# Kernel tuning notes

Measured on AMD Instinct MI355X. Metric: run time of the kernel, lower is better.

The kernel has to match this reference:

```python
import jax, jax.numpy as jnp
import numpy as np

HT_H, HT_W = 512, 512          # Hough accumulator grid
SPHERE_SIZE = 32768            # Gaussian-sphere bins
NUM_VOTES = 1_500_000          # rows in vote_mapping
BATCH, CHANNEL = 2, 64         # channel % 4 == 0 required by the module


def setup_inputs() -> dict:
    key = jax.random.key(0)
    k1, k2, k3, k4 = jax.random.split(key, 4)
    x = jax.random.normal(k1, (BATCH, CHANNEL, HT_H, HT_W), dtype=jnp.float32)
    ht_idx = jax.random.randint(k2, (NUM_VOTES,), 0, HT_H * HT_W, dtype=jnp.int32)
    sphere_idx = jax.random.randint(k3, (NUM_VOTES,), 0, SPHERE_SIZE, dtype=jnp.int32)
    weight = jax.random.uniform(k4, (NUM_VOTES,), dtype=jnp.float32)
    return {"x": x, "ht_idx": ht_idx, "sphere_idx": sphere_idx, "weight": weight}


def reference(x, ht_idx, sphere_idx, weight):
    b, c, h, w = x.shape
    # SPHERE_CUDA.forward: split channels into 4 groups, flatten HT grid
    xf = x.reshape(b * 4, c // 4, h * w)              # [B4, C4, HW]
    # HT2SPHERE: gather each vote's HT cell, scale by vote weight,
    # scatter-add into its sphere bin.
    votes = xf[:, :, ht_idx] * weight                  # [B4, C4, V]
    out = jax.ops.segment_sum(
        jnp.moveaxis(votes, -1, 0), sphere_idx, num_segments=SPHERE_SIZE
    )                                                  # [S, B4, C4]
    out = jnp.moveaxis(out, 0, -1)                     # [B4, C4, S]
    return out.reshape(b, c, SPHERE_SIZE)              # [B, C, S]
```

## Files before the change

### kernel.cpp

```cpp
#include <hip/hip_runtime.h>
#include <stdint.h>


#define S_BINS   32768
#define NBUCKET  1024
#define BINS     32
#define CAP      2048
#define CHUNK    8192
#define HT_BITS  18
#define CUR_STRIDE 16

__device__ __forceinline__ unsigned bf16_rne(float f) {
    unsigned u = __float_as_uint(f);
    return (u + 0x7FFFu + ((u >> 16) & 1u)) >> 16;
}

__global__ void init_kernel(int* __restrict__ cursor, int* __restrict__ spillCnt) {
    const int t = threadIdx.x;
    cursor[t * CUR_STRIDE] = t * CAP;
    if (t == 0) *spillCnt = 0;
}

__global__ __launch_bounds__(512) void fused_tr_kernel(
    const float* __restrict__ x, uint32_t* __restrict__ xTb, int HW,
    const int* __restrict__ ht, const int* __restrict__ sp,
    const float* __restrict__ w, int* __restrict__ cursor,
    uint2* __restrict__ records, uint2* __restrict__ spillRec,
    int* __restrict__ spillBkt, int* __restrict__ spillCnt,
    int V, int nrb) {
    __shared__ __align__(16) char smem[77888];
    const int t = threadIdx.x;
    if ((int)blockIdx.x < nrb) {
        uint2* rec   = (uint2*)smem;
        int*   hist  = (int*)(smem + 65536);
        int*   cur   = (int*)(smem + 69632);
        int*   gbase = (int*)(smem + 73728);
        int*   wsum  = (int*)(smem + 77824);
        const int blk = blockIdx.x;
        const int lane = t & 63, wv = t >> 6;
        const int base = blk * CHUNK, end = min(V, base + CHUNK), n = end - base;
        hist[2 * t] = 0; hist[2 * t + 1] = 0;
        __syncthreads();
        for (int v = base + t; v < end; v += 512) atomicAdd(&hist[sp[v] >> 5], 1);
        __syncthreads();
        const int l0 = hist[2 * t], l1 = hist[2 * t + 1];
        const int tot = l0 + l1;
        int sc = tot;
#pragma unroll
        for (int off = 1; off < 64; off <<= 1) {
            const int up = __shfl_up(sc, off);
            if (lane >= off) sc += up;
        }
        if (lane == 63) wsum[wv] = sc;
        __syncthreads();
        if (wv == 0 && lane < 8) {
            const int v0 = wsum[lane];
            int s = v0;
#pragma unroll
            for (int off = 1; off < 8; off <<= 1) {
                const int up = __shfl_up(s, off);
                if (lane >= off) s += up;
            }
            wsum[lane] = s - v0;
        }
        __syncthreads();
        const int run = wsum[wv] + (sc - tot);
        cur[2 * t]     = run;
        cur[2 * t + 1] = run + l0;
        if (l0) gbase[2 * t]     = atomicAdd(&cursor[(2 * t)     * CUR_STRIDE], l0);
        if (l1) gbase[2 * t + 1] = atomicAdd(&cursor[(2 * t + 1) * CUR_STRIDE], l1);
        __syncthreads();
        for (int v = base + t; v < end; v += 512) {
            const int s = sp[v];
            const int b = s >> 5, sl = s & 31;
            const int pos = atomicAdd(&cur[b], 1);
            rec[pos] = make_uint2((unsigned)ht[v] | ((unsigned)sl << HT_BITS),
                                  __float_as_uint(w[v]));
        }
        __syncthreads();
        for (int i = t; i < n; i += 512) {
            int lo = 0, hi = NBUCKET - 1;
#pragma unroll
            for (int it = 0; it < 10; ++it) {
                const int mid = (lo + hi) >> 1;
                if (i < cur[mid]) hi = mid; else lo = mid + 1;
            }
            const int b = lo;
            const int sb = (b == 0) ? 0 : cur[b - 1];
            const int slot = gbase[b] + (i - sb);
            if (slot < (b + 1) * CAP) {
                records[slot] = rec[i];
            } else {
                const int pos = atomicAdd(spillCnt, 1);
                spillRec[pos] = rec[i];
                spillBkt[pos] = b;
            }
        }
    } else {
        float* tile = (float*)smem;
        const int ht0 = ((int)blockIdx.x - nrb) * 64;
        for (int e = t; e < 128 * 64; e += 512) {
            const int ch = e >> 6, hl = e & 63;
            tile[hl * 129 + ch] = x[(size_t)ch * HW + ht0 + hl];
        }
        __syncthreads();
        for (int e = t; e < 64 * 64; e += 512) {
            const int hl = e >> 6, cp = e & 63;
            const unsigned lo = bf16_rne(tile[hl * 129 + cp]);
            const unsigned hi = bf16_rne(tile[hl * 129 + cp + 64]);
            xTb[(size_t)(ht0 + hl) * 64 + cp] = lo | (hi << 16);
        }
    }
}

__global__ __launch_bounds__(512) void accum_kernel(
    const uint32_t* __restrict__ xTb, const uint2* __restrict__ records,
    const int* __restrict__ cursor, const uint2* __restrict__ spillRec,
    const int* __restrict__ spillBkt, const int* __restrict__ spillCnt,
    float* __restrict__ out) {
    __shared__ uint2 sorted[CAP];
    __shared__ __align__(16) char rawbuf[BINS * 129 * 4];
    __shared__ int hist[BINS], off[BINS + 1], cur[BINS];
    uint2* raw = (uint2*)rawbuf;
    const uint4* xTb4 = (const uint4*)xTb;
    const int bkt = blockIdx.x, t = threadIdx.x;
    const int lane = t & 63, wv = t >> 6;
    const int q = lane >> 4, ql = lane & 15;
    const int n = min(cursor[bkt * CUR_STRIDE] - bkt * CAP, CAP);
    const int rbase = bkt * CAP;
    float a[4][8];
#pragma unroll
    for (int i = 0; i < 4; ++i)
#pragma unroll
        for (int j = 0; j < 8; ++j) a[i][j] = 0.f;

    if (t < BINS) hist[t] = 0;
    __syncthreads();
    for (int i = t; i < n; i += 512) {
        const uint2 r = records[rbase + i];
        raw[i] = r;
        atomicAdd(&hist[(r.x >> HT_BITS) & 31], 1);
    }
    __syncthreads();
    if (t == 0) {
        int run = 0;
        for (int j = 0; j < BINS; ++j) { off[j] = run; cur[j] = run; run += hist[j]; }
        off[BINS] = run;
    }
    __syncthreads();
    for (int i = t; i < n; i += 512) {
        const uint2 r = raw[i];
        const int pos = atomicAdd(&cur[(r.x >> HT_BITS) & 31], 1);
        sorted[pos] = r;
    }
    __syncthreads();
#pragma unroll
    for (int bb = 0; bb < 4; ++bb) {
        const int f = wv * 4 + bb;
        const int s0 = off[f], s1 = off[f + 1];
#pragma unroll 1
        for (int k = s0; k < s1; k += 16) {
#pragma unroll
            for (int u = 0; u < 4; ++u) {
                const int kk = k + 4 * u + q;
                if (kk < s1) {
                    const uint2 r = sorted[kk];
                    const uint4 g = xTb4[(size_t)(r.x & 0x3FFFF) * 16 + ql];
                    const float wt = __uint_as_float(r.y);
                    a[bb][0] += __uint_as_float(g.x << 16)          * wt;
                    a[bb][1] += __uint_as_float(g.x & 0xFFFF0000u)  * wt;
                    a[bb][2] += __uint_as_float(g.y << 16)          * wt;
                    a[bb][3] += __uint_as_float(g.y & 0xFFFF0000u)  * wt;
                    a[bb][4] += __uint_as_float(g.z << 16)          * wt;
                    a[bb][5] += __uint_as_float(g.z & 0xFFFF0000u)  * wt;
                    a[bb][6] += __uint_as_float(g.w << 16)          * wt;
                    a[bb][7] += __uint_as_float(g.w & 0xFFFF0000u)  * wt;
                }
            }
        }
    }
#pragma unroll
    for (int bb = 0; bb < 4; ++bb)
#pragma unroll
        for (int j = 0; j < 8; ++j) {
            a[bb][j] += __shfl_xor(a[bb][j], 16);
            a[bb][j] += __shfl_xor(a[bb][j], 32);
        }
    __syncthreads();
    float* epi = (float*)rawbuf;
    if (lane < 16) {
#pragma unroll
        for (int bb = 0; bb < 4; ++bb) {
            const int f = wv * 4 + bb;
            epi[f * 129 + 4 * ql]      = a[bb][0];
            epi[f * 129 + 4 * ql + 64] = a[bb][1];
            epi[f * 129 + 4 * ql + 1]  = a[bb][2];
            epi[f * 129 + 4 * ql + 65] = a[bb][3];
            epi[f * 129 + 4 * ql + 2]  = a[bb][4];
            epi[f * 129 + 4 * ql + 66] = a[bb][5];
            epi[f * 129 + 4 * ql + 3]  = a[bb][6];
            epi[f * 129 + 4 * ql + 67] = a[bb][7];
        }
    }
    __syncthreads();
    const int cnt = *spillCnt;
    if (cnt > 0) {
        const uint2* xTb2 = (const uint2*)xTb;
        const int hl = lane & 31;
        for (int i = t >> 5; i < cnt; i += 16) {
            if (spillBkt[i] == bkt) {
                const uint2 r = spillRec[i];
                const int f = (r.x >> HT_BITS) & 31;
                const uint2 g = xTb2[(size_t)(r.x & 0x3FFFF) * 32 + hl];
                const float wt = __uint_as_float(r.y);
                atomicAdd(&epi[f * 129 + 2 * hl],
                          __uint_as_float(g.x << 16) * wt);
                atomicAdd(&epi[f * 129 + 2 * hl + 64],
                          __uint_as_float(g.x & 0xFFFF0000u) * wt);
                atomicAdd(&epi[f * 129 + 2 * hl + 1],
                          __uint_as_float(g.y << 16) * wt);
                atomicAdd(&epi[f * 129 + 2 * hl + 65],
                          __uint_as_float(g.y & 0xFFFF0000u) * wt);
            }
        }
        __syncthreads();
    }
    for (int i = t; i < 128 * BINS; i += 512) {
        const int ch = i >> 5, bin = i & 31;
        out[(size_t)ch * S_BINS + bkt * BINS + bin] = epi[bin * 129 + ch];
    }
}

__global__ void direct_kernel(const float* __restrict__ x,
                              const int* __restrict__ ht_idx,
                              const int* __restrict__ sp_idx,
                              const float* __restrict__ weight,
                              float* __restrict__ out, int V, int HW, int S,
                              int CH) {
    const int v = blockIdx.x * 2 + (threadIdx.x >> 7);
    if (v >= V) return;
    const int ch = threadIdx.x & 127;
    if (ch >= CH) return;
    atomicAdd(&out[(size_t)ch * S + sp_idx[v]],
              x[(size_t)ch * HW + ht_idx[v]] * weight[v]);
}

extern "C" void kernel_launch(void* const* d_in, const int* in_sizes, int n_in,
                              void* d_out, int out_size, void* d_ws, size_t ws_size,
                              hipStream_t stream) {
    const float* x  = (const float*)d_in[0];
    const int*   ht = (const int*)d_in[1];
    const int*   sp = (const int*)d_in[2];
    const float* w  = (const float*)d_in[3];
    float* out = (float*)d_out;

    const int HW = 512 * 512;
    const int CH = in_sizes[0] / HW;
    const int S  = out_size / CH;
    const int V  = in_sizes[1];
    const int nrb = (V + CHUNK - 1) / CHUNK;
    const int ntb = HW / 64;

    const size_t xTb_bytes = (size_t)CH * HW * sizeof(uint16_t);
    const size_t rec_bytes = (size_t)NBUCKET * CAP * sizeof(uint2);
    const size_t spr_bytes = (size_t)V * sizeof(uint2);
    const size_t spb_bytes = (size_t)V * sizeof(int);
    const size_t cur_bytes = (size_t)NBUCKET * CUR_STRIDE * sizeof(int);
    const size_t cnt_bytes = 64;
    const size_t need = xTb_bytes + rec_bytes + spr_bytes + spb_bytes +
                        cur_bytes + cnt_bytes;

    if (CH == 128 && S == S_BINS && HW == (1 << HT_BITS) && ws_size >= need) {
        char* p = (char*)d_ws;
        uint32_t* xTb  = (uint32_t*)p;  p += xTb_bytes;
        uint2* records = (uint2*)p;     p += rec_bytes;
        uint2* spillRec= (uint2*)p;     p += spr_bytes;
        int* spillBkt  = (int*)p;       p += spb_bytes;
        int* cursor    = (int*)p;       p += cur_bytes;
        int* spillCnt  = (int*)p;

        init_kernel<<<1, NBUCKET, 0, stream>>>(cursor, spillCnt);
        fused_tr_kernel<<<nrb + ntb, 512, 0, stream>>>(
            x, xTb, HW, ht, sp, w, cursor, records, spillRec, spillBkt,
            spillCnt, V, nrb);
        accum_kernel<<<NBUCKET, 512, 0, stream>>>(xTb, records, cursor,
                                                  spillRec, spillBkt, spillCnt,
                                                  out);
    } else {
        hipMemsetAsync(out, 0, (size_t)out_size * sizeof(float), stream);
        direct_kernel<<<(V + 1) / 2, 256, 0, stream>>>(x, ht, sp, w, out, V, HW,
                                                       S, CH);
    }
}
```

Before: 299.4 us.

## Replace global bucket cursors with per-block sorted chunks gathered in accum

```diff
diff --git a/kernel.cpp b/kernel.cpp
--- a/kernel.cpp
+++ b/kernel.cpp
@@ -7,43 +7,34 @@
 #define BINS     32
 #define CAP      2048
 #define CHUNK    8192
+#define MAXRB    192
 #define HT_BITS  18
-#define CUR_STRIDE 16
 
 __device__ __forceinline__ unsigned bf16_rne(float f) {
     unsigned u = __float_as_uint(f);
     return (u + 0x7FFFu + ((u >> 16) & 1u)) >> 16;
 }
 
-__global__ void init_kernel(int* __restrict__ cursor, int* __restrict__ spillCnt) {
-    const int t = threadIdx.x;
-    cursor[t * CUR_STRIDE] = t * CAP;
-    if (t == 0) *spillCnt = 0;
-}
-
 __global__ __launch_bounds__(512) void fused_tr_kernel(
     const float* __restrict__ x, uint32_t* __restrict__ xTb, int HW,
     const int* __restrict__ ht, const int* __restrict__ sp,
-    const float* __restrict__ w, int* __restrict__ cursor,
-    uint2* __restrict__ records, uint2* __restrict__ spillRec,
-    int* __restrict__ spillBkt, int* __restrict__ spillCnt,
+    const float* __restrict__ w,
+    uint2* __restrict__ records, int* __restrict__ blkcur,
     int V, int nrb) {
-    __shared__ __align__(16) char smem[77888];
+    __shared__ __align__(16) char smem[69696];
     const int t = threadIdx.x;
     if ((int)blockIdx.x < nrb) {
-        uint2* rec   = (uint2*)smem;
-        int*   hist  = (int*)(smem + 65536);
-        int*   cur   = (int*)(smem + 69632);
-        int*   gbase = (int*)(smem + 73728);
-        int*   wsum  = (int*)(smem + 77824);
+        uint2* rec  = (uint2*)smem;
+        int*   hcur = (int*)(smem + 65536);
+        int*   wsum = (int*)(smem + 69632);
         const int blk = blockIdx.x;
         const int lane = t & 63, wv = t >> 6;
         const int base = blk * CHUNK, end = min(V, base + CHUNK), n = end - base;
-        hist[2 * t] = 0; hist[2 * t + 1] = 0;
-        __syncthreads();
-        for (int v = base + t; v < end; v += 512) atomicAdd(&hist[sp[v] >> 5], 1);
-        __syncthreads();
-        const int l0 = hist[2 * t], l1 = hist[2 * t + 1];
+        hcur[2 * t] = 0; hcur[2 * t + 1] = 0;
+        __syncthreads();
+        for (int v = base + t; v < end; v += 512) atomicAdd(&hcur[sp[v] >> 5], 1);
+        __syncthreads();
+        const int l0 = hcur[2 * t], l1 = hcur[2 * t + 1];
         const int tot = l0 + l1;
         int sc = tot;
 #pragma unroll
@@ -65,69 +56,59 @@
         }
         __syncthreads();
         const int run = wsum[wv] + (sc - tot);
-        cur[2 * t]     = run;
-        cur[2 * t + 1] = run + l0;
-        if (l0) gbase[2 * t]     = atomicAdd(&cursor[(2 * t)     * CUR_STRIDE], l0);
-        if (l1) gbase[2 * t + 1] = atomicAdd(&cursor[(2 * t + 1) * CUR_STRIDE], l1);
+        hcur[2 * t]     = run;
+        hcur[2 * t + 1] = run + l0;
         __syncthreads();
         for (int v = base + t; v < end; v += 512) {
             const int s = sp[v];
             const int b = s >> 5, sl = s & 31;
-            const int pos = atomicAdd(&cur[b], 1);
+            const int pos = atomicAdd(&hcur[b], 1);
             rec[pos] = make_uint2((unsigned)ht[v] | ((unsigned)sl << HT_BITS),
                                   __float_as_uint(w[v]));
         }
         __syncthreads();
-        for (int i = t; i < n; i += 512) {
-            int lo = 0, hi = NBUCKET - 1;
-#pragma unroll
-            for (int it = 0; it < 10; ++it) {
-                const int mid = (lo + hi) >> 1;
-                if (i < cur[mid]) hi = mid; else lo = mid + 1;
-            }
-            const int b = lo;
-            const int sb = (b == 0) ? 0 : cur[b - 1];
-            const int slot = gbase[b] + (i - sb);
-            if (slot < (b + 1) * CAP) {
-                records[slot] = rec[i];
-            } else {
-                const int pos = atomicAdd(spillCnt, 1);
-                spillRec[pos] = rec[i];
-                spillBkt[pos] = b;
-            }
-        }
+        for (int i = t; i < n; i += 512)
+            records[(size_t)blk * CHUNK + i] = rec[i];
+        blkcur[(size_t)blk * NBUCKET + 2 * t]     = hcur[2 * t];
+        blkcur[(size_t)blk * NBUCKET + 2 * t + 1] = hcur[2 * t + 1];
     } else {
         float* tile = (float*)smem;
         const int ht0 = ((int)blockIdx.x - nrb) * 64;
-        for (int e = t; e < 128 * 64; e += 512) {
-            const int ch = e >> 6, hl = e & 63;
-            tile[hl * 129 + ch] = x[(size_t)ch * HW + ht0 + hl];
-        }
-        __syncthreads();
-        for (int e = t; e < 64 * 64; e += 512) {
-            const int hl = e >> 6, cp = e & 63;
-            const unsigned lo = bf16_rne(tile[hl * 129 + cp]);
-            const unsigned hi = bf16_rne(tile[hl * 129 + cp + 64]);
-            xTb[(size_t)(ht0 + hl) * 64 + cp] = lo | (hi << 16);
+        for (int e = t; e < 128 * 16; e += 512) {
+            const int ch = e >> 4, hq = e & 15;
+            const float4 v = *(const float4*)(x + (size_t)ch * HW + ht0 + 4 * hq);
+            const int a = 4 * hq;
+            tile[(a + 0) * 129 + ch] = v.x;
+            tile[(a + 1) * 129 + ch] = v.y;
+            tile[(a + 2) * 129 + ch] = v.z;
+            tile[(a + 3) * 129 + ch] = v.w;
+        }
+        __syncthreads();
+        for (int e = t; e < 64 * 32; e += 512) {
+            const int hl = e >> 5, cp = (e & 31) * 2;
+            const unsigned lo0 = bf16_rne(tile[hl * 129 + cp]);
+            const unsigned hi0 = bf16_rne(tile[hl * 129 + cp + 64]);
+            const unsigned lo1 = bf16_rne(tile[hl * 129 + cp + 1]);
+            const unsigned hi1 = bf16_rne(tile[hl * 129 + cp + 65]);
+            *(uint2*)(xTb + (size_t)(ht0 + hl) * 64 + cp) =
+                make_uint2(lo0 | (hi0 << 16), lo1 | (hi1 << 16));
         }
     }
 }
 
 __global__ __launch_bounds__(512) void accum_kernel(
     const uint32_t* __restrict__ xTb, const uint2* __restrict__ records,
-    const int* __restrict__ cursor, const uint2* __restrict__ spillRec,
-    const int* __restrict__ spillBkt, const int* __restrict__ spillCnt,
-    float* __restrict__ out) {
+    const int* __restrict__ blkcur, int nrb, float* __restrict__ out) {
     __shared__ uint2 sorted[CAP];
     __shared__ __align__(16) char rawbuf[BINS * 129 * 4];
     __shared__ int hist[BINS], off[BINS + 1], cur[BINS];
+    __shared__ int segcnt[MAXRB], segpos[MAXRB];
+    __shared__ int ntot;
     uint2* raw = (uint2*)rawbuf;
     const uint4* xTb4 = (const uint4*)xTb;
     const int bkt = blockIdx.x, t = threadIdx.x;
     const int lane = t & 63, wv = t >> 6;
     const int q = lane >> 4, ql = lane & 15;
-    const int n = min(cursor[bkt * CUR_STRIDE] - bkt * CAP, CAP);
-    const int rbase = bkt * CAP;
     float a[4][8];
 #pragma unroll
     for (int i = 0; i < 4; ++i)
@@ -135,11 +116,43 @@
         for (int j = 0; j < 8; ++j) a[i][j] = 0.f;
 
     if (t < BINS) hist[t] = 0;
-    __syncthreads();
-    for (int i = t; i < n; i += 512) {
-        const uint2 r = records[rbase + i];
-        raw[i] = r;
-        atomicAdd(&hist[(r.x >> HT_BITS) & 31], 1);
+    int s0 = 0;
+    if (t < nrb) {
+        const int e1 = blkcur[(size_t)t * NBUCKET + bkt];
+        s0 = (bkt == 0) ? 0 : blkcur[(size_t)t * NBUCKET + bkt - 1];
+        segcnt[t] = e1 - s0;
+    }
+    __syncthreads();
+    if (wv == 0) {
+        int carry = 0;
+        for (int b0 = 0; b0 < nrb; b0 += 64) {
+            const int idx = b0 + lane;
+            const int c = (idx < nrb) ? segcnt[idx] : 0;
+            int sc = c;
+#pragma unroll
+            for (int off2 = 1; off2 < 64; off2 <<= 1) {
+                const int up = __shfl_up(sc, off2);
+                if (lane >= off2) sc += up;
+            }
+            if (idx < nrb) segpos[idx] = carry + sc - c;
+            carry += __shfl(sc, 63);
+        }
+        if (lane == 0) ntot = carry;
+    }
+    __syncthreads();
+    const int n = min(ntot, CAP);
+    if (t < nrb) {
+        const int cnt = segcnt[t];
+        const int p = segpos[t];
+        const uint2* src = records + (size_t)t * CHUNK + s0;
+        for (int j = 0; j < cnt; ++j) {
+            const int d = p + j;
+            if (d < CAP) {
+                const uint2 r = src[j];
+                raw[d] = r;
+                atomicAdd(&hist[(r.x >> HT_BITS) & 31], 1);
+            }
+        }
     }
     __syncthreads();
     if (t == 0) {
@@ -157,13 +170,13 @@
 #pragma unroll
     for (int bb = 0; bb < 4; ++bb) {
         const int f = wv * 4 + bb;
-        const int s0 = off[f], s1 = off[f + 1];
+        const int s0f = off[f], s1f = off[f + 1];
 #pragma unroll 1
-        for (int k = s0; k < s1; k += 16) {
+        for (int k = s0f; k < s1f; k += 16) {
 #pragma unroll
             for (int u = 0; u < 4; ++u) {
                 const int kk = k + 4 * u + q;
-                if (kk < s1) {
+                if (kk < s1f) {
                     const uint2 r = sorted[kk];
                     const uint4 g = xTb4[(size_t)(r.x & 0x3FFFF) * 16 + ql];
                     const float wt = __uint_as_float(r.y);
@@ -203,28 +216,6 @@
         }
     }
     __syncthreads();
-    const int cnt = *spillCnt;
-    if (cnt > 0) {
-        const uint2* xTb2 = (const uint2*)xTb;
-        const int hl = lane & 31;
-        for (int i = t >> 5; i < cnt; i += 16) {
-            if (spillBkt[i] == bkt) {
-                const uint2 r = spillRec[i];
-                const int f = (r.x >> HT_BITS) & 31;
-                const uint2 g = xTb2[(size_t)(r.x & 0x3FFFF) * 32 + hl];
-                const float wt = __uint_as_float(r.y);
-                atomicAdd(&epi[f * 129 + 2 * hl],
-                          __uint_as_float(g.x << 16) * wt);
-                atomicAdd(&epi[f * 129 + 2 * hl + 64],
-                          __uint_as_float(g.x & 0xFFFF0000u) * wt);
-                atomicAdd(&epi[f * 129 + 2 * hl + 1],
-                          __uint_as_float(g.y << 16) * wt);
-                atomicAdd(&epi[f * 129 + 2 * hl + 65],
-                          __uint_as_float(g.y & 0xFFFF0000u) * wt);
-            }
-        }
-        __syncthreads();
-    }
     for (int i = t; i < 128 * BINS; i += 512) {
         const int ch = i >> 5, bin = i & 31;
         out[(size_t)ch * S_BINS + bkt * BINS + bin] = epi[bin * 129 + ch];
@@ -262,29 +253,20 @@
     const int ntb = HW / 64;
 
     const size_t xTb_bytes = (size_t)CH * HW * sizeof(uint16_t);
-    const size_t rec_bytes = (size_t)NBUCKET * CAP * sizeof(uint2);
-    const size_t spr_bytes = (size_t)V * sizeof(uint2);
-    const size_t spb_bytes = (size_t)V * sizeof(int);
-    const size_t cur_bytes = (size_t)NBUCKET * CUR_STRIDE * sizeof(int);
-    const size_t cnt_bytes = 64;
-    const size_t need = xTb_bytes + rec_bytes + spr_bytes + spb_bytes +
-                        cur_bytes + cnt_bytes;
-
-    if (CH == 128 && S == S_BINS && HW == (1 << HT_BITS) && ws_size >= need) {
+    const size_t rec_bytes = (size_t)MAXRB * CHUNK * sizeof(uint2);
+    const size_t cur_bytes = (size_t)MAXRB * NBUCKET * sizeof(int);
+    const size_t need = xTb_bytes + rec_bytes + cur_bytes;
+
+    if (CH == 128 && S == S_BINS && HW == (1 << HT_BITS) && nrb <= MAXRB &&
+        ws_size >= need) {
         char* p = (char*)d_ws;
         uint32_t* xTb  = (uint32_t*)p;  p += xTb_bytes;
         uint2* records = (uint2*)p;     p += rec_bytes;
-        uint2* spillRec= (uint2*)p;     p += spr_bytes;
-        int* spillBkt  = (int*)p;       p += spb_bytes;
-        int* cursor    = (int*)p;       p += cur_bytes;
-        int* spillCnt  = (int*)p;
-
-        init_kernel<<<1, NBUCKET, 0, stream>>>(cursor, spillCnt);
+        int* blkcur    = (int*)p;
+
         fused_tr_kernel<<<nrb + ntb, 512, 0, stream>>>(
-            x, xTb, HW, ht, sp, w, cursor, records, spillRec, spillBkt,
-            spillCnt, V, nrb);
-        accum_kernel<<<NBUCKET, 512, 0, stream>>>(xTb, records, cursor,
-                                                  spillRec, spillBkt, spillCnt,
+            x, xTb, HW, ht, sp, w, records, blkcur, V, nrb);
+        accum_kernel<<<NBUCKET, 512, 0, stream>>>(xTb, records, blkcur, nrb,
                                                   out);
     } else {
         hipMemsetAsync(out, 0, (size_t)out_size * sizeof(float), stream);
```

New measurement: 303.0 us. No clear change (+1.2%).
